# Kernel tuning notes

Hardware: AMD Instinct MI355X
Metric: run time of the kernel (lower is better)

## Reference

```python
import jax, jax.numpy as jnp
import numpy as np

HARMONICS = 5


def _harmonic_basis(x):
    k = jnp.arange(1, HARMONICS + 1, dtype=x.dtype)            # [H]
    kx = x[..., None] * k                                       # [B, D, H]
    sc = jnp.stack([jnp.sin(kx), jnp.cos(kx)], axis=-1)         # [B, D, H, 2]
    sc = sc.reshape(*x.shape, 2 * HARMONICS)                    # interleaved sin/cos
    ones = jnp.ones((*x.shape, 1), dtype=x.dtype)
    return jnp.concatenate([ones, sc], axis=-1)                 # [B, D, 2H+1]


def setup_inputs() -> dict:
    key = jax.random.key(0)
    k1, k2, k3 = jax.random.split(key, 3)
    B, D, F, H = 16384, 256, 11, 256
    x = jax.random.normal(k1, (B, D), dtype=jnp.float32)
    W = jax.random.normal(k2, (D, F, H), dtype=jnp.float32) * (1.0 / np.sqrt(F))
    b = jax.random.normal(k3, (D, H), dtype=jnp.float32) * 0.01
    return {"x": x, "W": W, "b": b}


def reference(x, W, b) -> jnp.ndarray:
    # basis expansion per feature, batched small GEMM, summed over features
    basis = _harmonic_basis(x)                                  # [B, D, F]
    out = jnp.einsum('bdf,dfh->bh', basis, W)                   # sum over features fused
    out = out + jnp.sum(b, axis=0)                              # sum of per-feature biases
    return out
```

## Files before the change

### kernel.cpp

```cpp
#include <hip/hip_runtime.h>
#include <hip/hip_bf16.h>


#define BDIM 16384
#define DDIM 256
#define HOUT 256
#define KTOT 2560
#define NKT  80
#define BM 64
#define BN 128

typedef __bf16 bf16x8 __attribute__((ext_vector_type(8)));
typedef float floatx4 __attribute__((ext_vector_type(4)));

__device__ __forceinline__ unsigned short f2bf(float f) {
    unsigned int u = __float_as_uint(f);
    return (unsigned short)((u + 0x7FFFu + ((u >> 16) & 1u)) >> 16);
}

__device__ __forceinline__ unsigned int pkbf(float a, float b) {
    __hip_bfloat162 r = __float22bfloat162_rn(make_float2(a, b));
    return *reinterpret_cast<unsigned int*>(&r);
}

__global__ void prep_kernel(const float* __restrict__ W, const float* __restrict__ bias,
                            unsigned short* __restrict__ Wfrag, float* __restrict__ c_part) {
    const int bid = blockIdx.x;
    const int t = threadIdx.x;
    if (bid < NKT) {
        const int kt = bid;
        const int dtile = kt / 10;
        const int f = kt - dtile * 10 + 1;
        const float* wsrc = W + ((size_t)(dtile * 32) * 11 + f) * 256 + t;
        union { unsigned short s[32]; int4 v[4]; } buf;
#pragma unroll
        for (int dd = 0; dd < 32; ++dd)
            buf.s[dd] = f2bf(wsrc[(size_t)dd * 11 * 256]);
        int4* dst = (int4*)(Wfrag + ((size_t)kt * 256 + t) * 32);
#pragma unroll
        for (int v = 0; v < 4; ++v) dst[v] = buf.v[v];
    } else {
        const int p = bid - NKT;
        float acc = 0.f;
#pragma unroll
        for (int dd = 0; dd < 32; ++dd) {
            const int d = p * 32 + dd;
            acc += W[(size_t)(d * 11) * 256 + t] + bias[(size_t)d * 256 + t];
        }
        c_part[p * 256 + t] = acc;
    }
}

__global__ __launch_bounds__(256, 2)
void kan_gemm(const float* __restrict__ x, const unsigned short* __restrict__ Wfrag,
              const float* __restrict__ c_part, float* __restrict__ out) {
    __shared__ unsigned short As[10 * 4 * 512];

    const int t = threadIdx.x;
    const int m0 = blockIdx.x * BM;
    const int h0 = blockIdx.y * BN;

    const int lane = t & 63;
    const int wave = t >> 6;
    const int wr = wave >> 1;
    const int wc = wave & 1;
    const int l15 = lane & 15;
    const int koff = lane >> 4;

    const int m_a = lane;
    const int q = wave;
    const int it_w = m_a >> 4;
    const int slot = (m_a & 15) + 16 * q;

    floatx4 acc[2][4];
#pragma unroll
    for (int i = 0; i < 2; ++i)
#pragma unroll
        for (int j = 0; j < 4; ++j)
            acc[i][j] = (floatx4){0.f, 0.f, 0.f, 0.f};

    const float* xrow = x + (size_t)(m0 + m_a) * DDIM;
    const unsigned short* bbase = Wfrag + (size_t)(h0 + wc * 64 + l15) * 32 + koff * 8;

    float4 xa = *(const float4*)(xrow + q * 8);
    float4 xb = *(const float4*)(xrow + q * 8 + 4);

    for (int dtile = 0; dtile < 8; ++dtile) {
        float xv[8] = {xa.x, xa.y, xa.z, xa.w, xb.x, xb.y, xb.z, xb.w};
        float sc[8], cc[8], sp[8], cp[8], t2c[8];
#pragma unroll
        for (int j = 0; j < 8; ++j) {
            __sincosf(xv[j], &sc[j], &cc[j]);
            t2c[j] = cc[j] + cc[j];
            sp[j] = 0.f;
            cp[j] = 1.f;
        }
#pragma unroll
        for (int k = 1; k <= 5; ++k) {
            union { unsigned int u[4]; int4 v; } vs, vc;
#pragma unroll
            for (int p = 0; p < 4; ++p) {
                vs.u[p] = pkbf(sc[2 * p], sc[2 * p + 1]);
                vc.u[p] = pkbf(cc[2 * p], cc[2 * p + 1]);
            }
            *(int4*)(&As[((2 * k - 2) * 4 + it_w) * 512 + slot * 8]) = vs.v;
            *(int4*)(&As[((2 * k - 1) * 4 + it_w) * 512 + slot * 8]) = vc.v;
            if (k < 5) {
#pragma unroll
                for (int j = 0; j < 8; ++j) {
                    const float ns = t2c[j] * sc[j] - sp[j];
                    const float nc = t2c[j] * cc[j] - cp[j];
                    sp[j] = sc[j]; cp[j] = cc[j];
                    sc[j] = ns;   cc[j] = nc;
                }
            }
        }
        __syncthreads();

        if (dtile < 7) {
            xa = *(const float4*)(xrow + (dtile + 1) * 32 + q * 8);
            xb = *(const float4*)(xrow + (dtile + 1) * 32 + q * 8 + 4);
        }

        const unsigned short* bkt = bbase + (size_t)(dtile * 10) * 8192;

        bf16x8 bf0[4], bf1[4], af0[2], af1[2];
#pragma unroll
        for (int j = 0; j < 4; ++j)
            bf0[j] = *(const bf16x8*)(bkt + j * 512);
#pragma unroll
        for (int i = 0; i < 2; ++i)
            af0[i] = *(const bf16x8*)(&As[(0 * 4 + wr * 2 + i) * 512 + lane * 8]);

#pragma unroll
        for (int hs = 0; hs < 10; ++hs) {
            bf16x8* bnext = (hs & 1) ? bf0 : bf1;
            bf16x8* anext = (hs & 1) ? af0 : af1;
            if (hs < 9) {
#pragma unroll
                for (int j = 0; j < 4; ++j)
                    bnext[j] = *(const bf16x8*)(bkt + (size_t)(hs + 1) * 8192 + j * 512);
#pragma unroll
                for (int i = 0; i < 2; ++i)
                    anext[i] = *(const bf16x8*)(&As[((hs + 1) * 4 + wr * 2 + i) * 512 + lane * 8]);
            }
            const bf16x8* bcur = (hs & 1) ? bf1 : bf0;
            const bf16x8* acur = (hs & 1) ? af1 : af0;
#pragma unroll
            for (int i = 0; i < 2; ++i)
#pragma unroll
                for (int j = 0; j < 4; ++j)
                    acc[i][j] = __builtin_amdgcn_mfma_f32_16x16x32_bf16(acur[i], bcur[j], acc[i][j], 0, 0, 0);
        }
        __syncthreads();
    }

    float cj[4];
#pragma unroll
    for (int j = 0; j < 4; ++j) {
        const int col = h0 + wc * 64 + j * 16 + l15;
        float s = 0.f;
#pragma unroll
        for (int p = 0; p < 8; ++p) s += c_part[p * 256 + col];
        cj[j] = s;
    }
#pragma unroll
    for (int i = 0; i < 2; ++i) {
        const int row0 = m0 + wr * 32 + i * 16 + koff * 4;
#pragma unroll
        for (int j = 0; j < 4; ++j) {
            const int col = h0 + wc * 64 + j * 16 + l15;
#pragma unroll
            for (int r = 0; r < 4; ++r)
                out[(size_t)(row0 + r) * HOUT + col] = acc[i][j][r] + cj[j];
        }
    }
}

extern "C" void kernel_launch(void* const* d_in, const int* in_sizes, int n_in,
                              void* d_out, int out_size, void* d_ws, size_t ws_size,
                              hipStream_t stream) {
    const float* x = (const float*)d_in[0];
    const float* W = (const float*)d_in[1];
    const float* b = (const float*)d_in[2];
    float* out = (float*)d_out;

    unsigned short* Wfrag = (unsigned short*)d_ws;
    float* c_part = (float*)((char*)d_ws + (size_t)NKT * 256 * 32 * 2);

    prep_kernel<<<NKT + 8, 256, 0, stream>>>(W, b, Wfrag, c_part);
    kan_gemm<<<dim3(BDIM / BM, HOUT / BN), 256, 0, stream>>>(x, Wfrag, c_part, out);
}
```

Before: 116.3 us.

## Double-buffer LDS basis tile and deepen register prefetch of W fragments

The shared basis buffer becomes double-buffered by dtile parity, which removes the trailing barrier in each iteration. The B-fragment prefetch is now a 5-deep rotating register ring that carries across dtile boundaries, and the A fragments use a 3-deep ring. The goal is to hide global-load latency for W and cut barrier stalls. In exchange it doubles LDS usage to 80KB per block and adds register pressure (20 bf16x8 B regs), which could hurt occupancy under launch_bounds(256,2). One write-after-read hazard on the alternate buffer still relies on the single remaining barrier.

Result: faster. 113.5 us (-2.4%).

```diff
diff --git a/kernel.cpp b/kernel.cpp
--- a/kernel.cpp
+++ b/kernel.cpp
@@ -54,7 +54,7 @@
 __global__ __launch_bounds__(256, 2)
 void kan_gemm(const float* __restrict__ x, const unsigned short* __restrict__ Wfrag,
               const float* __restrict__ c_part, float* __restrict__ out) {
-    __shared__ unsigned short As[10 * 4 * 512];
+    __shared__ unsigned short As[2][10 * 4 * 512];
 
     const int t = threadIdx.x;
     const int m0 = blockIdx.x * BM;
@@ -85,7 +85,16 @@
     float4 xa = *(const float4*)(xrow + q * 8);
     float4 xb = *(const float4*)(xrow + q * 8 + 4);
 
+    bf16x8 bf[5][4];
+#pragma unroll
+    for (int p = 0; p < 5; ++p)
+#pragma unroll
+        for (int j = 0; j < 4; ++j)
+            bf[p][j] = *(const bf16x8*)(bbase + (size_t)p * 8192 + j * 512);
+
     for (int dtile = 0; dtile < 8; ++dtile) {
+        unsigned short* asb = &As[dtile & 1][0];
+
         float xv[8] = {xa.x, xa.y, xa.z, xa.w, xb.x, xb.y, xb.z, xb.w};
         float sc[8], cc[8], sp[8], cp[8], t2c[8];
 #pragma unroll
@@ -103,8 +112,8 @@
                 vs.u[p] = pkbf(sc[2 * p], sc[2 * p + 1]);
                 vc.u[p] = pkbf(cc[2 * p], cc[2 * p + 1]);
             }
-            *(int4*)(&As[((2 * k - 2) * 4 + it_w) * 512 + slot * 8]) = vs.v;
-            *(int4*)(&As[((2 * k - 1) * 4 + it_w) * 512 + slot * 8]) = vc.v;
+            *(int4*)(&asb[((2 * k - 2) * 4 + it_w) * 512 + slot * 8]) = vs.v;
+            *(int4*)(&asb[((2 * k - 1) * 4 + it_w) * 512 + slot * 8]) = vc.v;
             if (k < 5) {
 #pragma unroll
                 for (int j = 0; j < 8; ++j) {
@@ -122,37 +131,34 @@
             xb = *(const float4*)(xrow + (dtile + 1) * 32 + q * 8 + 4);
         }
 
-        const unsigned short* bkt = bbase + (size_t)(dtile * 10) * 8192;
-
-        bf16x8 bf0[4], bf1[4], af0[2], af1[2];
+        bf16x8 af[3][2];
 #pragma unroll
-        for (int j = 0; j < 4; ++j)
-            bf0[j] = *(const bf16x8*)(bkt + j * 512);
+        for (int p = 0; p < 3; ++p)
 #pragma unroll
-        for (int i = 0; i < 2; ++i)
-            af0[i] = *(const bf16x8*)(&As[(0 * 4 + wr * 2 + i) * 512 + lane * 8]);
+            for (int i = 0; i < 2; ++i)
+                af[p][i] = *(const bf16x8*)(&asb[(p * 4 + wr * 2 + i) * 512 + lane * 8]);
 
 #pragma unroll
         for (int hs = 0; hs < 10; ++hs) {
-            bf16x8* bnext = (hs & 1) ? bf0 : bf1;
-            bf16x8* anext = (hs & 1) ? af0 : af1;
-            if (hs < 9) {
-#pragma unroll
-                for (int j = 0; j < 4; ++j)
-                    bnext[j] = *(const bf16x8*)(bkt + (size_t)(hs + 1) * 8192 + j * 512);
-#pragma unroll
-                for (int i = 0; i < 2; ++i)
-                    anext[i] = *(const bf16x8*)(&As[((hs + 1) * 4 + wr * 2 + i) * 512 + lane * 8]);
-            }
-            const bf16x8* bcur = (hs & 1) ? bf1 : bf0;
-            const bf16x8* acur = (hs & 1) ? af1 : af0;
 #pragma unroll
             for (int i = 0; i < 2; ++i)
 #pragma unroll
                 for (int j = 0; j < 4; ++j)
-                    acc[i][j] = __builtin_amdgcn_mfma_f32_16x16x32_bf16(acur[i], bcur[j], acc[i][j], 0, 0, 0);
+                    acc[i][j] = __builtin_amdgcn_mfma_f32_16x16x32_bf16(af[hs % 3][i], bf[hs % 5][j], acc[i][j], 0, 0, 0);
+
+            {
+                int ktp = dtile * 10 + hs + 5;
+                if (ktp > 79) ktp = 79;
+#pragma unroll
+                for (int j = 0; j < 4; ++j)
+                    bf[hs % 5][j] = *(const bf16x8*)(bbase + (size_t)ktp * 8192 + j * 512);
+            }
+            if (hs < 7) {
+#pragma unroll
+                for (int i = 0; i < 2; ++i)
+                    af[hs % 3][i] = *(const bf16x8*)(&asb[((hs + 3) * 4 + wr * 2 + i) * 512 + lane * 8]);
+            }
         }
-        __syncthreads();
     }
 
     float cj[4];
```
